# Kernel optimization log

Measured on AMD Instinct MI355X. Metric: run time of the kernel, lower is better.

Reference implementation:

```python
import jax, jax.numpy as jnp
import numpy as np

B, T, D, H = 2, 2048, 1024, 16
DH = D // H


def setup_inputs() -> dict:
    key = jax.random.key(0)
    k1, k2, k3 = jax.random.split(key, 3)
    x = jax.random.normal(k1, (B, T, D), dtype=jnp.float32)
    # causal mask: True at positions to mask (strict upper triangle)
    attn_mask = jnp.triu(jnp.ones((T, T), dtype=bool), k=1)
    attn_mask = jnp.broadcast_to(attn_mask, (B, T, T))
    Wqkv = jax.random.normal(k2, (D, 3 * D), dtype=jnp.float32) * (D ** -0.5)
    Wo = jax.random.normal(k3, (D, D), dtype=jnp.float32) * (D ** -0.5)
    bo = jnp.zeros((D,), dtype=jnp.float32)
    return {"x": x, "attn_mask": attn_mask, "Wqkv": Wqkv, "Wo": Wo, "bo": bo}


def reference(x, attn_mask, Wqkv, Wo, bo):
    # qkv projection (bias=False), split into q,k,v like torch chunk(3, dim=-1)
    qkv = x @ Wqkv                                  # [B,T,3D]
    q, k, v = jnp.split(qkv, 3, axis=-1)            # each [B,T,D]
    q = q.reshape(B, T, H, DH).transpose(0, 2, 1, 3)  # [B,H,T,DH]
    k = k.reshape(B, T, H, DH).transpose(0, 2, 1, 3)
    v = v.reshape(B, T, H, DH).transpose(0, 2, 1, 3)
    scores = jnp.einsum('bhqd,bhkd->bhqk', q, k) / jnp.sqrt(jnp.float32(DH))
    scores = jnp.where(attn_mask[:, None, :, :], -jnp.inf, scores)
    weights = jax.nn.softmax(scores, axis=-1)       # [B,H,T,T]
    out = jnp.einsum('bhqk,bhkd->bhqd', weights, v)  # [B,H,T,DH]
    out = out.transpose(0, 2, 1, 3).reshape(B, T, D)
    out = out @ Wo + bo                              # o_proj
    # dropout is identity in eval mode
    return (out, weights)
```

## Files before the change

### kernel.cpp

```cpp
#include <hip/hip_runtime.h>
#include <hip/hip_bf16.h>


typedef __attribute__((ext_vector_type(8))) short short8;
typedef __attribute__((ext_vector_type(4))) float floatx4;

typedef __attribute__((address_space(1))) const unsigned int gas_u32;
typedef __attribute__((address_space(3))) unsigned int las_u32;

__device__ inline void gl16(const void* g, void* l) {
  __builtin_amdgcn_global_load_lds((gas_u32*)g, (las_u32*)l, 16, 0, 0);
}

__device__ inline unsigned short f2bf(float f) {
  union { float f; unsigned u; } x; x.f = f;
  unsigned r = x.u + 0x7fffu + ((x.u >> 16) & 1u);
  return (unsigned short)(r >> 16);
}

__global__ __launch_bounds__(256) void convert_x_kernel(
    const float* __restrict__ src, unsigned short* __restrict__ dst, int n4) {
  int i = blockIdx.x * 256 + threadIdx.x;
  int stride = gridDim.x * 256;
  for (; i < n4; i += stride) {
    float4 v = ((const float4*)src)[i];
    ushort4 o;
    o.x = f2bf(v.x); o.y = f2bf(v.y); o.z = f2bf(v.z); o.w = f2bf(v.w);
    ((ushort4*)dst)[i] = o;
  }
}

__global__ __launch_bounds__(256) void tconv_kernel(
    const float* __restrict__ src, unsigned short* __restrict__ dst,
    int R, int C) {
  __shared__ float tile[32][33];
  int c0 = blockIdx.x * 32, r0 = blockIdx.y * 32;
  int tr = threadIdx.x >> 5, tc = threadIdx.x & 31;
#pragma unroll
  for (int i = 0; i < 4; ++i) {
    int r = tr + i * 8;
    tile[r][tc] = src[(size_t)(r0 + r) * C + c0 + tc];
  }
  __syncthreads();
#pragma unroll
  for (int i = 0; i < 4; ++i) {
    int r = tr + i * 8;
    dst[(size_t)(c0 + r) * R + r0 + tc] = f2bf(tile[tc][r]);
  }
}

__global__ __launch_bounds__(256) void gemm_qkv_kernel(
    const unsigned short* __restrict__ A,
    const unsigned short* __restrict__ Bt,
    unsigned short* __restrict__ qb, unsigned short* __restrict__ kb,
    unsigned short* __restrict__ vtb) {
  __shared__ __align__(16) unsigned short As[128][32];
  __shared__ __align__(16) unsigned short Bs[128][32];
  const int tid = threadIdx.x;
  const int w = tid >> 6, lane = tid & 63, quad = lane >> 4, l15 = lane & 15;
  const int wm = (w >> 1) * 64, wn = (w & 1) * 64;
  const int m0 = blockIdx.y * 128, n0 = blockIdx.x * 128;
  floatx4 acc[4][4] = {};
  for (int k0 = 0; k0 < 1024; k0 += 32) {
    __syncthreads();
#pragma unroll
    for (int it = 0; it < 2; ++it) {
      int s = tid + it * 256;
      int r = s >> 2, seg = s & 3;
      gl16(A + (size_t)(m0 + r) * 1024 + k0 + seg * 8, &As[r][seg * 8]);
      gl16(Bt + (size_t)(n0 + r) * 1024 + k0 + seg * 8, &Bs[r][seg * 8]);
    }
    __syncthreads();
    short8 a[4], b[4];
#pragma unroll
    for (int i = 0; i < 4; ++i) a[i] = *(const short8*)&As[wm + i * 16 + l15][quad * 8];
#pragma unroll
    for (int j = 0; j < 4; ++j) b[j] = *(const short8*)&Bs[wn + j * 16 + l15][quad * 8];
#pragma unroll
    for (int i = 0; i < 4; ++i)
#pragma unroll
      for (int j = 0; j < 4; ++j)
        acc[i][j] = __builtin_amdgcn_mfma_f32_16x16x32_bf16(a[i], b[j], acc[i][j], 0, 0, 0);
  }
  const int sel = n0 >> 10;
#pragma unroll
  for (int i = 0; i < 4; ++i) {
    int m = m0 + wm + i * 16 + quad * 4;
    int bb = m >> 11, t = m & 2047;
    if (sel < 2) {
      unsigned short* dst = (sel == 0) ? qb : kb;
#pragma unroll
      for (int j = 0; j < 4; ++j) {
        int n = n0 + wn + j * 16 + l15;
        int h = (n & 1023) >> 6, dh = n & 63;
        int bh = bb * 16 + h;
#pragma unroll
        for (int r = 0; r < 4; ++r) {
          int trow = t + r;
          int swdh = ((((dh >> 3) ^ (trow & 7)) << 3)) | (dh & 7);
          dst[((size_t)bh * 2048 + trow) * 64 + swdh] = f2bf(acc[i][j][r]);
        }
      }
    } else {
#pragma unroll
      for (int j = 0; j < 4; ++j) {
        int n = n0 + wn + j * 16 + l15;
        int h = (n & 1023) >> 6, dh = n & 63;
        int bh = bb * 16 + h;
        ushort4 p;
        p.x = f2bf(acc[i][j][0]); p.y = f2bf(acc[i][j][1]);
        p.z = f2bf(acc[i][j][2]); p.w = f2bf(acc[i][j][3]);
        int swoff = (((((t & 63) >> 3) ^ (dh & 7)) << 3)) | (t & 7);
        *(ushort4*)&vtb[((size_t)bh * 64 + dh) * 2048 + (t & ~63) + swoff] = p;
      }
    }
  }
}

__global__ __launch_bounds__(256) void attn_kernel(
    const unsigned short* __restrict__ qb, const unsigned short* __restrict__ kb,
    const unsigned short* __restrict__ vtb,
    float* __restrict__ wout,
    unsigned short* __restrict__ attnb) {
  __shared__ __align__(16) unsigned short Qs[64][64];
  __shared__ __align__(16) unsigned short Ks[64][64];
  __shared__ __align__(16) unsigned short Vs[64][64];
  __shared__ __align__(16) unsigned short Es[64][64];
  const int tid = threadIdx.x;
  const int w = tid >> 6, lane = tid & 63, quad = lane >> 4, l15 = lane & 15;
  const int bh = blockIdx.x >> 4;
  const int j = blockIdx.x & 15;
  const size_t kvbase = (size_t)bh * 131072;
  const int key = l15 & 7;
  const int rowb = w * 16 + quad * 4;

  for (int half = 0; half < 2; ++half) {
    const int qt = half ? j : (31 - j);

    {
      int nz4 = (31 - qt) * 16;
      if (nz4 > 0) {
        floatx4 z4 = {0.f, 0.f, 0.f, 0.f};
        floatx4* wbase = (floatx4*)(wout + ((size_t)(bh * 2048 + qt * 64)) * 2048 + (qt + 1) * 64);
        for (int r = 0; r < 64; ++r) {
          floatx4* row = wbase + (size_t)r * 512;
          for (int c4 = tid; c4 < nz4; c4 += 256)
            __builtin_nontemporal_store(z4, row + c4);
        }
      }
    }
#pragma unroll
    for (int it = 0; it < 2; ++it) {
      int s = tid + it * 256, r = s >> 3, c8 = s & 7;
      gl16(qb + kvbase + (size_t)(qt * 64 + r) * 64 + c8 * 8, &Qs[r][c8 * 8]);
    }
    __syncthreads();
    const short8 aq0 = *(const short8*)&Qs[w * 16 + l15][(quad ^ key) << 3];
    const short8 aq1 = *(const short8*)&Qs[w * 16 + l15][((quad + 4) ^ key) << 3];

    float sums[4] = {0.f, 0.f, 0.f, 0.f};
    for (int kt = 0; kt <= qt; ++kt) {
      __syncthreads();
#pragma unroll
      for (int it = 0; it < 2; ++it) {
        int s = tid + it * 256, r = s >> 3, c8 = s & 7;
        gl16(kb + kvbase + (size_t)(kt * 64 + r) * 64 + c8 * 8, &Ks[r][c8 * 8]);
      }
      __syncthreads();
#pragma unroll
      for (int c = 0; c < 4; ++c) {
        short8 b0 = *(const short8*)&Ks[c * 16 + l15][(quad ^ key) << 3];
        short8 b1 = *(const short8*)&Ks[c * 16 + l15][((quad + 4) ^ key) << 3];
        floatx4 d = {0.f, 0.f, 0.f, 0.f};
        d = __builtin_amdgcn_mfma_f32_16x16x32_bf16(aq0, b0, d, 0, 0, 0);
        d = __builtin_amdgcn_mfma_f32_16x16x32_bf16(aq1, b1, d, 0, 0, 0);
        int col = c * 16 + l15;
        if (kt == qt) {
#pragma unroll
          for (int r = 0; r < 4; ++r)
            sums[r] += (col <= rowb + r) ? __expf(d[r] * 0.125f) : 0.f;
        } else {
#pragma unroll
          for (int r = 0; r < 4; ++r) sums[r] += __expf(d[r] * 0.125f);
        }
      }
    }
    float rinv[4];
#pragma unroll
    for (int r = 0; r < 4; ++r) {
      float s = sums[r];
      s += __shfl_xor(s, 1); s += __shfl_xor(s, 2);
      s += __shfl_xor(s, 4); s += __shfl_xor(s, 8);
      rinv[r] = 1.f / s;
    }

    floatx4 oacc[4] = {};
    const size_t wrowbase = ((size_t)(bh * 2048 + qt * 64 + rowb)) * 2048;
    for (int kt = 0; kt <= qt; ++kt) {
      __syncthreads();
#pragma unroll
      for (int it = 0; it < 2; ++it) {
        int s = tid + it * 256, r = s >> 3, c8 = s & 7;
        gl16(kb + kvbase + (size_t)(kt * 64 + r) * 64 + c8 * 8, &Ks[r][c8 * 8]);
        gl16(vtb + kvbase + (size_t)r * 2048 + kt * 64 + c8 * 8, &Vs[r][c8 * 8]);
      }
      __syncthreads();
#pragma unroll
      for (int c = 0; c < 4; ++c) {
        short8 b0 = *(const short8*)&Ks[c * 16 + l15][(quad ^ key) << 3];
        short8 b1 = *(const short8*)&Ks[c * 16 + l15][((quad + 4) ^ key) << 3];
        floatx4 d = {0.f, 0.f, 0.f, 0.f};
        d = __builtin_amdgcn_mfma_f32_16x16x32_bf16(aq0, b0, d, 0, 0, 0);
        d = __builtin_amdgcn_mfma_f32_16x16x32_bf16(aq1, b1, d, 0, 0, 0);
        int col = c * 16 + l15;
#pragma unroll
        for (int r = 0; r < 4; ++r) {
          float ev = __expf(d[r] * 0.125f);
          if (kt == qt && col > rowb + r) ev = 0.f;
          __builtin_nontemporal_store(ev * rinv[r],
              wout + wrowbase + (size_t)r * 2048 + kt * 64 + col);
          int erow = rowb + r;
          int sc = (((col >> 3) ^ (erow & 7)) << 3) | (col & 7);
          Es[erow][sc] = f2bf(ev);
        }
      }
      const short8 ae0 = *(const short8*)&Es[w * 16 + l15][(quad ^ key) << 3];
      const short8 ae1 = *(const short8*)&Es[w * 16 + l15][((quad + 4) ^ key) << 3];
#pragma unroll
      for (int c = 0; c < 4; ++c) {
        short8 bv0 = *(const short8*)&Vs[c * 16 + l15][(quad ^ key) << 3];
        short8 bv1 = *(const short8*)&Vs[c * 16 + l15][((quad + 4) ^ key) << 3];
        oacc[c] = __builtin_amdgcn_mfma_f32_16x16x32_bf16(ae0, bv0, oacc[c], 0, 0, 0);
        oacc[c] = __builtin_amdgcn_mfma_f32_16x16x32_bf16(ae1, bv1, oacc[c], 0, 0, 0);
      }
    }
    const int bb = bh >> 4, h = bh & 15;
#pragma unroll
    for (int c = 0; c < 4; ++c)
#pragma unroll
      for (int r = 0; r < 4; ++r) {
        int q = qt * 64 + w * 16 + quad * 4 + r;
        attnb[((size_t)bb * 2048 + q) * 1024 + h * 64 + c * 16 + l15] =
            f2bf(oacc[c][r] * rinv[r]);
      }
  }
}

__global__ __launch_bounds__(256) void gemm_o_kernel(
    const unsigned short* __restrict__ A,
    const unsigned short* __restrict__ Bt,
    const float* __restrict__ bo,
    float* __restrict__ out) {
  __shared__ __align__(16) unsigned short As[128][32];
  __shared__ __align__(16) unsigned short Bs[128][32];
  const int tid = threadIdx.x;
  const int w = tid >> 6, lane = tid & 63, quad = lane >> 4, l15 = lane & 15;
  const int wm = (w >> 1) * 64, wn = (w & 1) * 64;
  const int m0 = blockIdx.y * 128, n0 = blockIdx.x * 128;
  floatx4 acc[4][4] = {};
  for (int k0 = 0; k0 < 1024; k0 += 32) {
    __syncthreads();
#pragma unroll
    for (int it = 0; it < 2; ++it) {
      int s = tid + it * 256;
      int r = s >> 2, seg = s & 3;
      gl16(A + (size_t)(m0 + r) * 1024 + k0 + seg * 8, &As[r][seg * 8]);
      gl16(Bt + (size_t)(n0 + r) * 1024 + k0 + seg * 8, &Bs[r][seg * 8]);
    }
    __syncthreads();
    short8 a[4], b[4];
#pragma unroll
    for (int i = 0; i < 4; ++i) a[i] = *(const short8*)&As[wm + i * 16 + l15][quad * 8];
#pragma unroll
    for (int j = 0; j < 4; ++j) b[j] = *(const short8*)&Bs[wn + j * 16 + l15][quad * 8];
#pragma unroll
    for (int i = 0; i < 4; ++i)
#pragma unroll
      for (int j = 0; j < 4; ++j)
        acc[i][j] = __builtin_amdgcn_mfma_f32_16x16x32_bf16(a[i], b[j], acc[i][j], 0, 0, 0);
  }
#pragma unroll
  for (int i = 0; i < 4; ++i) {
    int m = m0 + wm + i * 16 + quad * 4;
#pragma unroll
    for (int j = 0; j < 4; ++j) {
      int n = n0 + wn + j * 16 + l15;
      float bias = bo[n];
#pragma unroll
      for (int r = 0; r < 4; ++r)
        out[(size_t)(m + r) * 1024 + n] = acc[i][j][r] + bias;
    }
  }
}

extern "C" void kernel_launch(void* const* d_in, const int* in_sizes, int n_in,
                              void* d_out, int out_size, void* d_ws, size_t ws_size,
                              hipStream_t stream) {
  const float* x    = (const float*)d_in[0];
  const float* wqkv = (const float*)d_in[2];
  const float* wo   = (const float*)d_in[3];
  const float* bo   = (const float*)d_in[4];
  float* out  = (float*)d_out;
  float* wout = out + 4194304;

  unsigned short* xb    = (unsigned short*)d_ws;
  unsigned short* wqkvT = xb + 4194304;
  unsigned short* woT   = wqkvT + 3145728;
  unsigned short* qb    = woT + 1048576;
  unsigned short* kb    = qb + 4194304;
  unsigned short* vtb   = kb + 4194304;
  unsigned short* attnb = vtb + 4194304;

  convert_x_kernel<<<1024, 256, 0, stream>>>(x, xb, 1048576);
  tconv_kernel<<<dim3(96, 32), 256, 0, stream>>>(wqkv, wqkvT, 1024, 3072);
  tconv_kernel<<<dim3(32, 32), 256, 0, stream>>>(wo, woT, 1024, 1024);
  gemm_qkv_kernel<<<dim3(24, 32), 256, 0, stream>>>(xb, wqkvT, qb, kb, vtb);
  attn_kernel<<<512, 256, 0, stream>>>(qb, kb, vtb, wout, attnb);
  gemm_o_kernel<<<dim3(8, 32), 256, 0, stream>>>(attnb, woT, bo, out);
}
```

Before: 755.9 us.

## Double-buffer K/V tiles in attention loops with async prefetch

```diff
diff --git a/kernel.cpp b/kernel.cpp
--- a/kernel.cpp
+++ b/kernel.cpp
@@ -123,8 +123,8 @@
     float* __restrict__ wout,
     unsigned short* __restrict__ attnb) {
   __shared__ __align__(16) unsigned short Qs[64][64];
-  __shared__ __align__(16) unsigned short Ks[64][64];
-  __shared__ __align__(16) unsigned short Vs[64][64];
+  __shared__ __align__(16) unsigned short Ks[2][64][64];
+  __shared__ __align__(16) unsigned short Vs[2][64][64];
   __shared__ __align__(16) unsigned short Es[64][64];
   const int tid = threadIdx.x;
   const int w = tid >> 6, lane = tid & 63, quad = lane >> 4, l15 = lane & 15;
@@ -133,6 +133,17 @@
   const size_t kvbase = (size_t)bh * 131072;
   const int key = l15 & 7;
   const int rowb = w * 16 + quad * 4;
+  const int sr0 = tid >> 3, sc0 = (tid & 7) * 8;
+  const int sr1 = sr0 + 32;
+
+  auto stage_k = [&](int kt, int buf) {
+    gl16(kb + kvbase + (size_t)(kt * 64 + sr0) * 64 + sc0, &Ks[buf][sr0][sc0]);
+    gl16(kb + kvbase + (size_t)(kt * 64 + sr1) * 64 + sc0, &Ks[buf][sr1][sc0]);
+  };
+  auto stage_v = [&](int kt, int buf) {
+    gl16(vtb + kvbase + (size_t)sr0 * 2048 + kt * 64 + sc0, &Vs[buf][sr0][sc0]);
+    gl16(vtb + kvbase + (size_t)sr1 * 2048 + kt * 64 + sc0, &Vs[buf][sr1][sc0]);
+  };
 
   for (int half = 0; half < 2; ++half) {
     const int qt = half ? j : (31 - j);
@@ -149,28 +160,22 @@
         }
       }
     }
-#pragma unroll
-    for (int it = 0; it < 2; ++it) {
-      int s = tid + it * 256, r = s >> 3, c8 = s & 7;
-      gl16(qb + kvbase + (size_t)(qt * 64 + r) * 64 + c8 * 8, &Qs[r][c8 * 8]);
-    }
+    gl16(qb + kvbase + (size_t)(qt * 64 + sr0) * 64 + sc0, &Qs[sr0][sc0]);
+    gl16(qb + kvbase + (size_t)(qt * 64 + sr1) * 64 + sc0, &Qs[sr1][sc0]);
+    stage_k(0, 0);
     __syncthreads();
     const short8 aq0 = *(const short8*)&Qs[w * 16 + l15][(quad ^ key) << 3];
     const short8 aq1 = *(const short8*)&Qs[w * 16 + l15][((quad + 4) ^ key) << 3];
 
     float sums[4] = {0.f, 0.f, 0.f, 0.f};
+    int cur = 0;
     for (int kt = 0; kt <= qt; ++kt) {
-      __syncthreads();
-#pragma unroll
-      for (int it = 0; it < 2; ++it) {
-        int s = tid + it * 256, r = s >> 3, c8 = s & 7;
-        gl16(kb + kvbase + (size_t)(kt * 64 + r) * 64 + c8 * 8, &Ks[r][c8 * 8]);
-      }
-      __syncthreads();
+      if (kt < qt) stage_k(kt + 1, cur ^ 1);
+      __builtin_amdgcn_s_setprio(1);
 #pragma unroll
       for (int c = 0; c < 4; ++c) {
-        short8 b0 = *(const short8*)&Ks[c * 16 + l15][(quad ^ key) << 3];
-        short8 b1 = *(const short8*)&Ks[c * 16 + l15][((quad + 4) ^ key) << 3];
+        short8 b0 = *(const short8*)&Ks[cur][c * 16 + l15][(quad ^ key) << 3];
+        short8 b1 = *(const short8*)&Ks[cur][c * 16 + l15][((quad + 4) ^ key) << 3];
         floatx4 d = {0.f, 0.f, 0.f, 0.f};
         d = __builtin_amdgcn_mfma_f32_16x16x32_bf16(aq0, b0, d, 0, 0, 0);
         d = __builtin_amdgcn_mfma_f32_16x16x32_bf16(aq1, b1, d, 0, 0, 0);
@@ -184,6 +189,9 @@
           for (int r = 0; r < 4; ++r) sums[r] += __expf(d[r] * 0.125f);
         }
       }
+      __builtin_amdgcn_s_setprio(0);
+      __syncthreads();
+      cur ^= 1;
     }
     float rinv[4];
 #pragma unroll
@@ -196,19 +204,17 @@
 
     floatx4 oacc[4] = {};
     const size_t wrowbase = ((size_t)(bh * 2048 + qt * 64 + rowb)) * 2048;
+    stage_k(0, 0);
+    stage_v(0, 0);
+    __syncthreads();
+    cur = 0;
     for (int kt = 0; kt <= qt; ++kt) {
-      __syncthreads();
-#pragma unroll
-      for (int it = 0; it < 2; ++it) {
-        int s = tid + it * 256, r = s >> 3, c8 = s & 7;
-        gl16(kb + kvbase + (size_t)(kt * 64 + r) * 64 + c8 * 8, &Ks[r][c8 * 8]);
-        gl16(vtb + kvbase + (size_t)r * 2048 + kt * 64 + c8 * 8, &Vs[r][c8 * 8]);
-      }
-      __syncthreads();
+      if (kt < qt) { stage_k(kt + 1, cur ^ 1); stage_v(kt + 1, cur ^ 1); }
+      __builtin_amdgcn_s_setprio(1);
 #pragma unroll
       for (int c = 0; c < 4; ++c) {
-        short8 b0 = *(const short8*)&Ks[c * 16 + l15][(quad ^ key) << 3];
-        short8 b1 = *(const short8*)&Ks[c * 16 + l15][((quad + 4) ^ key) << 3];
+        short8 b0 = *(const short8*)&Ks[cur][c * 16 + l15][(quad ^ key) << 3];
+        short8 b1 = *(const short8*)&Ks[cur][c * 16 + l15][((quad + 4) ^ key) << 3];
         floatx4 d = {0.f, 0.f, 0.f, 0.f};
         d = __builtin_amdgcn_mfma_f32_16x16x32_bf16(aq0, b0, d, 0, 0, 0);
         d = __builtin_amdgcn_mfma_f32_16x16x32_bf16(aq1, b1, d, 0, 0, 0);
@@ -228,11 +234,14 @@
       const short8 ae1 = *(const short8*)&Es[w * 16 + l15][((quad + 4) ^ key) << 3];
 #pragma unroll
       for (int c = 0; c < 4; ++c) {
-        short8 bv0 = *(const short8*)&Vs[c * 16 + l15][(quad ^ key) << 3];
-        short8 bv1 = *(const short8*)&Vs[c * 16 + l15][((quad + 4) ^ key) << 3];
+        short8 bv0 = *(const short8*)&Vs[cur][c * 16 + l15][(quad ^ key) << 3];
+        short8 bv1 = *(const short8*)&Vs[cur][c * 16 + l15][((quad + 4) ^ key) << 3];
         oacc[c] = __builtin_amdgcn_mfma_f32_16x16x32_bf16(ae0, bv0, oacc[c], 0, 0, 0);
         oacc[c] = __builtin_amdgcn_mfma_f32_16x16x32_bf16(ae1, bv1, oacc[c], 0, 0, 0);
       }
+      __builtin_amdgcn_s_setprio(0);
+      __syncthreads();
+      cur ^= 1;
     }
     const int bb = bh >> 4, h = bh & 15;
 #pragma unroll
```

Result: no change. 750.6 us (-0.7%).
